# Kernel tuning notes

Measured on AMD Instinct MI355X. Metric: run time of the kernel, lower is better.

The kernel has to match this reference:

```python
import jax, jax.numpy as jnp
import numpy as np

B, N, DIN, D, L, H = 8, 1024, 768, 384, 6, 12
HD = D // H
STD = 0.02
EPS = 1e-5


def setup_inputs() -> dict:
    key = jax.random.key(0)
    ks = jax.random.split(key, 24)
    inp = {}
    inp["x"] = jax.random.normal(ks[0], (B, N, DIN), jnp.float32)
    inp["height_ids"] = jax.random.randint(ks[1], (B, N), 0, 48)
    inp["width_ids"] = jax.random.randint(ks[2], (B, N), 0, 48)
    inp["target_mask"] = jax.random.randint(ks[3], (B, N), 0, 2).astype(bool)
    inp["sequence_ids"] = jnp.sort(jax.random.randint(ks[4], (B, N), 0, 8), axis=-1)
    inp["sequence_mask"] = (jax.random.randint(ks[5], (B, N), 0, 10) > 8)
    inp["r"] = 0
    # parameters (weights stored [in, out]; y = x @ W + b)
    inp["embed_w"] = jax.random.normal(ks[6], (DIN, D), jnp.float32) * STD
    inp["embed_b"] = jnp.zeros((D,), jnp.float32)
    inp["h_embed"] = jax.random.normal(ks[7], (48, D), jnp.float32) * STD
    inp["w_embed"] = jax.random.normal(ks[8], (48, D), jnp.float32) * STD
    inp["mask_token"] = jax.random.normal(ks[9], (D,), jnp.float32) * STD
    rescale = (1.0 / jnp.sqrt(2.0 * (jnp.arange(L) + 1.0))).astype(jnp.float32)
    inp["norm1_w"] = jnp.ones((L, D), jnp.float32)
    inp["norm1_b"] = jnp.zeros((L, D), jnp.float32)
    inp["ls1"] = 1e-5 * jnp.ones((L, D), jnp.float32)
    inp["qkv_w"] = jax.random.normal(ks[10], (L, D, 3 * D), jnp.float32) * STD
    inp["qkv_b"] = jnp.zeros((L, 3 * D), jnp.float32)
    inp["proj_w"] = jax.random.normal(ks[11], (L, D, D), jnp.float32) * STD * rescale[:, None, None]
    inp["proj_b"] = jnp.zeros((L, D), jnp.float32)
    inp["norm2_w"] = jnp.ones((L, D), jnp.float32)
    inp["norm2_b"] = jnp.zeros((L, D), jnp.float32)
    inp["fc1_w"] = jax.random.normal(ks[12], (L, D, 4 * D), jnp.float32) * STD
    inp["fc1_b"] = jnp.zeros((L, 4 * D), jnp.float32)
    inp["fc2_w"] = jax.random.normal(ks[13], (L, 4 * D, D), jnp.float32) * STD * rescale[:, None, None]
    inp["fc2_b"] = jnp.zeros((L, D), jnp.float32)
    inp["ls2"] = 1e-5 * jnp.ones((L, D), jnp.float32)
    inp["pnorm_w"] = jnp.ones((D,), jnp.float32)
    inp["pnorm_b"] = jnp.zeros((D,), jnp.float32)
    inp["pproj_w"] = jax.random.normal(ks[14], (D, DIN), jnp.float32) * STD
    inp["pproj_b"] = jnp.zeros((DIN,), jnp.float32)
    return inp


def _layernorm(x, w, b):
    mu = jnp.mean(x, axis=-1, keepdims=True)
    var = jnp.mean(jnp.square(x - mu), axis=-1, keepdims=True)
    return (x - mu) * jax.lax.rsqrt(var + EPS) * w + b


def _attention(x, attn_mask, qkv_w, qkv_b, proj_w, proj_b):
    # x: [B,N,D]; attn_mask: [B,1,N,N] True where attention is disallowed
    qkv = (x @ qkv_w + qkv_b).reshape(B, N, 3, H, HD).transpose(2, 0, 3, 1, 4)
    q, k, v = qkv[0], qkv[1], qkv[2]  # [B,H,N,HD]
    attn = jnp.einsum("bhnd,bhmd->bhnm", q, k) * (HD ** -0.5)
    neg_inf = jnp.finfo(attn.dtype).min
    attn = jnp.where(attn_mask, neg_inf, attn)
    attn = jax.nn.softmax(attn, axis=-1)
    out = jnp.einsum("bhnm,bhmd->bhnd", attn, v).transpose(0, 2, 1, 3).reshape(B, N, D)
    return out @ proj_w + proj_b


def reference(x, height_ids, width_ids, target_mask, sequence_ids, sequence_mask, r,
              embed_w, embed_b, h_embed, w_embed, mask_token,
              norm1_w, norm1_b, ls1, qkv_w, qkv_b, proj_w, proj_b,
              norm2_w, norm2_b, fc1_w, fc1_b, fc2_w, fc2_b, ls2,
              pnorm_w, pnorm_b, pproj_w, pproj_b):
    h = x @ embed_w + embed_b
    tm = target_mask[..., None]
    h = jnp.where(tm, mask_token, h)
    h = h + h_embed[height_ids] + w_embed[width_ids]
    # packed-sequence block-diagonal mask; True = NOT allowed
    mask = sequence_ids[:, :, None] != sequence_ids[:, None, :]
    mask = mask | sequence_mask[:, :, None] | sequence_mask[:, None, :]
    mask = mask[:, None]  # broadcast over heads: [B,1,N,N]
    for i in range(L):  # r == 0 path: plain blocks, tome is None
        h = h + ls1[i] * _attention(_layernorm(h, norm1_w[i], norm1_b[i]), mask,
                                    qkv_w[i], qkv_b[i], proj_w[i], proj_b[i])
        z = _layernorm(h, norm2_w[i], norm2_b[i])
        z = jax.nn.gelu(z @ fc1_w[i] + fc1_b[i], approximate=False) @ fc2_w[i] + fc2_b[i]
        h = h + ls2[i] * z
    h = _layernorm(h, pnorm_w, pnorm_b)
    return h @ pproj_w + pproj_b
```

## Files before the change

### kernel.cpp

```cpp
#include <hip/hip_runtime.h>
#include <math.h>

#define BB   8
#define NN   1024
#define DIN  768
#define DD   384
#define LL   6
#define HH   12
#define HDD  32
#define MM   (BB*NN)
#define EPSF 1e-5f

typedef __attribute__((ext_vector_type(8))) short short8;
typedef __attribute__((ext_vector_type(4))) float f32x4;

__device__ __forceinline__ unsigned short f2b(float f) {
    unsigned int u = __builtin_bit_cast(unsigned int, f);
    u = (u + 0x7fffu + ((u >> 16) & 1u)) >> 16;
    return (unsigned short)u;
}
__device__ __forceinline__ float b2f(unsigned short h) {
    return __builtin_bit_cast(float, ((unsigned int)h) << 16);
}

__global__ __launch_bounds__(1024) void cvt_mask_k(const void* __restrict__ src,
                                                   int n, int* __restrict__ dst)
{
    __shared__ int flag;
    if (threadIdx.x == 0) flag = 0;
    __syncthreads();
    const int* si = (const int*)src;
    int nq = n >> 2;
    int any = 0;
    for (int i = threadIdx.x; i < nq; i += blockDim.x) any |= si[i] & ~1;
    if (any) atomicOr(&flag, 1);
    __syncthreads();
    if (flag) {
        const unsigned char* sb = (const unsigned char*)src;
        for (int i = threadIdx.x; i < n; i += blockDim.x) dst[i] = sb[i];
    } else {
        for (int i = threadIdx.x; i < n; i += blockDim.x) dst[i] = si[i];
    }
}

__global__ __launch_bounds__(64) void kminmax_k(const int* __restrict__ sids,
                                                const int* __restrict__ smask,
                                                int2* __restrict__ kmm)
{
    int e = blockIdx.x;
    int b = e >> 4, kt = e & 15;
    int lane = threadIdx.x;
    int kk = b * NN + kt * 64 + lane;
    int s = sids[kk];
    int msk = smask[kk];
    int mn = msk ? 0x7fffffff : s;
    int mx = msk ? (int)0x80000000 : s;
    #pragma unroll
    for (int off = 32; off; off >>= 1) {
        mn = min(mn, __shfl_xor(mn, off));
        mx = max(mx, __shfl_xor(mx, off));
    }
    if (lane == 0) kmm[e] = make_int2(mn, mx);
}

__global__ __launch_bounds__(256) void vmean_k(const unsigned short* __restrict__ qkv,
                                               unsigned short* __restrict__ vmean)
{
    __shared__ float part[8][32];
    int bh = blockIdx.x;
    int b = bh / HH, h = bh % HH;
    int d = threadIdx.x & 31, grp = threadIdx.x >> 5;
    const unsigned short* vp = qkv + (size_t)(b * NN + grp * 128) * (3 * DD)
                                   + 2 * DD + h * HDD + d;
    float s = 0.f;
    for (int n = 0; n < 128; ++n)
        s += b2f(vp[(size_t)n * 3 * DD]);
    part[grp][d] = s;
    __syncthreads();
    if (grp == 0) {
        float t = 0.f;
        #pragma unroll
        for (int g2 = 0; g2 < 8; ++g2) t += part[g2][d];
        vmean[bh * HDD + d] = f2b(t * (1.0f / NN));
    }
}

__global__ __launch_bounds__(256) void tcast_k(const float* __restrict__ W,
                                               unsigned short* __restrict__ Wt,
                                               int K, int N)
{
    __shared__ float tile[32][33];
    const size_t lstr = (size_t)K * N;
    const float* Wl = W + blockIdx.z * lstr;
    unsigned short* Wtl = Wt + blockIdx.z * lstr;
    int k0 = blockIdx.x * 32, n0 = blockIdx.y * 32;
    int tx = threadIdx.x & 31, ty = threadIdx.x >> 5;
    #pragma unroll
    for (int r = 0; r < 32; r += 8)
        tile[ty + r][tx] = Wl[(size_t)(k0 + ty + r) * N + n0 + tx];
    __syncthreads();
    #pragma unroll
    for (int r = 0; r < 32; r += 8)
        Wtl[(size_t)(n0 + ty + r) * K + k0 + tx] = f2b(tile[tx][ty + r]);
}

__global__ __launch_bounds__(256) void tcast2_k(const float* __restrict__ W,
                                                unsigned short* __restrict__ WTh,
                                                unsigned short* __restrict__ WTl,
                                                int K, int N)
{
    __shared__ float tile[32][33];
    int k0 = blockIdx.x * 32, n0 = blockIdx.y * 32;
    int tx = threadIdx.x & 31, ty = threadIdx.x >> 5;
    #pragma unroll
    for (int r = 0; r < 32; r += 8)
        tile[ty + r][tx] = W[(size_t)(k0 + ty + r) * N + n0 + tx];
    __syncthreads();
    #pragma unroll
    for (int r = 0; r < 32; r += 8) {
        float v = tile[tx][ty + r];
        unsigned short hi = f2b(v);
        unsigned short lo = f2b(v - b2f(hi));
        size_t idx = (size_t)(n0 + ty + r) * K + k0 + tx;
        WTh[idx] = hi;
        WTl[idx] = lo;
    }
}

template <int EPI>
__global__ __launch_bounds__(256) void sgemm_k(
    const float* __restrict__ A,
    const unsigned short* __restrict__ WTh, const unsigned short* __restrict__ WTl,
    const float* __restrict__ bias, float* __restrict__ out,
    int K, int NO,
    const int* __restrict__ tmask, const int* __restrict__ hids,
    const int* __restrict__ wids, const float* __restrict__ mtok,
    const float* __restrict__ hemb, const float* __restrict__ wemb)
{
    __shared__ unsigned short Ah[128][40];
    __shared__ unsigned short Al[128][40];
    __shared__ unsigned short Bh[64][40];
    __shared__ unsigned short Bl[64][40];

    const int tid  = threadIdx.x;
    const int lane = tid & 63;
    const int wave = tid >> 6;
    const int wr = wave >> 1, wc = wave & 1;
    const int rowBase = blockIdx.x * 128;
    const int colBase = blockIdx.y * 64;
    const int rr = lane & 15;
    const int kr = (lane >> 4) * 8;

    f32x4 acc[4][2] = {};

    for (int k0 = 0; k0 < K; k0 += 32) {
        #pragma unroll
        for (int i = 0; i < 4; ++i) {
            int s   = tid + i * 256;
            int row = s >> 3;
            int q   = (s & 7) * 4;
            float4 av = *(const float4*)&A[(size_t)(rowBase + row) * K + k0 + q];
            ushort4 h4, l4;
            #pragma unroll
            for (int e = 0; e < 4; ++e) {
                float v = ((const float*)&av)[e];
                unsigned short hi = f2b(v);
                ((unsigned short*)&h4)[e] = hi;
                ((unsigned short*)&l4)[e] = f2b(v - b2f(hi));
            }
            *(ushort4*)&Ah[row][q] = h4;
            *(ushort4*)&Al[row][q] = l4;
        }
        {
            int s   = tid;
            int row = s >> 2;
            int seg = (s & 3) * 8;
            size_t gi = (size_t)(colBase + row) * K + k0 + seg;
            *(short8*)&Bh[row][seg] = *(const short8*)&WTh[gi];
            *(short8*)&Bl[row][seg] = *(const short8*)&WTl[gi];
        }
        __syncthreads();

        short8 ah[4], al[4], bh2[2], bl2[2];
        #pragma unroll
        for (int i = 0; i < 4; ++i) {
            ah[i] = *(const short8*)&Ah[wr * 64 + i * 16 + rr][kr];
            al[i] = *(const short8*)&Al[wr * 64 + i * 16 + rr][kr];
        }
        #pragma unroll
        for (int j = 0; j < 2; ++j) {
            bh2[j] = *(const short8*)&Bh[wc * 32 + j * 16 + rr][kr];
            bl2[j] = *(const short8*)&Bl[wc * 32 + j * 16 + rr][kr];
        }
        #pragma unroll
        for (int i = 0; i < 4; ++i)
            #pragma unroll
            for (int j = 0; j < 2; ++j) {
                acc[i][j] = __builtin_amdgcn_mfma_f32_16x16x32_bf16(
                    al[i], bh2[j], acc[i][j], 0, 0, 0);
                acc[i][j] = __builtin_amdgcn_mfma_f32_16x16x32_bf16(
                    ah[i], bl2[j], acc[i][j], 0, 0, 0);
                acc[i][j] = __builtin_amdgcn_mfma_f32_16x16x32_bf16(
                    ah[i], bh2[j], acc[i][j], 0, 0, 0);
            }
        __syncthreads();
    }

    const int colq = colBase + wc * 32 + rr;
    const int rq0  = rowBase + wr * 64 + (lane >> 4) * 4;
    #pragma unroll
    for (int j = 0; j < 2; ++j) {
        const int col = colq + j * 16;
        const float bi = bias[col];
        #pragma unroll
        for (int i = 0; i < 4; ++i) {
            #pragma unroll
            for (int r = 0; r < 4; ++r) {
                const int row = rq0 + i * 16 + r;
                float v = acc[i][j][r] + bi;
                if constexpr (EPI == 1) {
                    float xv = tmask[row] ? mtok[col] : v;
                    out[(size_t)row * NO + col] = xv
                        + hemb[(size_t)hids[row] * DD + col]
                        + wemb[(size_t)wids[row] * DD + col];
                } else {
                    out[(size_t)row * NO + col] = v;
                }
            }
        }
    }
}

template <int EPI>
__global__ __launch_bounds__(256) void bgemm_k(
    const unsigned short* __restrict__ A, const unsigned short* __restrict__ Wt,
    const float* __restrict__ bias, void* __restrict__ out,
    int K, int NO, const float* __restrict__ ls)
{
    __shared__ unsigned short As[128][40];
    __shared__ unsigned short Bs[128][40];

    const int tid  = threadIdx.x;
    const int lane = tid & 63;
    const int wave = tid >> 6;
    const int wr = wave >> 1, wc = wave & 1;
    const int rowBase = blockIdx.x * 128;
    const int colBase = blockIdx.y * 128;
    const int rr = lane & 15;
    const int kr = (lane >> 4) * 8;

    f32x4 acc[4][4] = {};

    for (int k0 = 0; k0 < K; k0 += 32) {
        #pragma unroll
        for (int i = 0; i < 2; ++i) {
            int s   = tid + i * 256;
            int row = s >> 2;
            int seg = (s & 3) * 8;
            *(short8*)&As[row][seg] =
                *(const short8*)&A[(size_t)(rowBase + row) * K + k0 + seg];
            *(short8*)&Bs[row][seg] =
                *(const short8*)&Wt[(size_t)(colBase + row) * K + k0 + seg];
        }
        __syncthreads();

        short8 af[4], bfr[4];
        #pragma unroll
        for (int i = 0; i < 4; ++i)
            af[i] = *(const short8*)&As[wr * 64 + i * 16 + rr][kr];
        #pragma unroll
        for (int j = 0; j < 4; ++j)
            bfr[j] = *(const short8*)&Bs[wc * 64 + j * 16 + rr][kr];
        #pragma unroll
        for (int i = 0; i < 4; ++i)
            #pragma unroll
            for (int j = 0; j < 4; ++j)
                acc[i][j] = __builtin_amdgcn_mfma_f32_16x16x32_bf16(
                    af[i], bfr[j], acc[i][j], 0, 0, 0);
        __syncthreads();
    }

    const int colq = colBase + wc * 64 + rr;
    const int rq0  = rowBase + wr * 64 + (lane >> 4) * 4;
    #pragma unroll
    for (int j = 0; j < 4; ++j) {
        const int col = colq + j * 16;
        const float bi = bias[col];
        float lsv = 0.f;
        if constexpr (EPI == 2) lsv = ls[col];
        #pragma unroll
        for (int i = 0; i < 4; ++i) {
            #pragma unroll
            for (int r = 0; r < 4; ++r) {
                const int row = rq0 + i * 16 + r;
                float v = acc[i][j][r] + bi;
                if constexpr (EPI == 0) {
                    ((unsigned short*)out)[(size_t)row * NO + col] = f2b(v);
                } else if constexpr (EPI == 2) {
                    float* hp = (float*)out + (size_t)row * NO + col;
                    *hp += lsv * v;
                } else {
                    float g = 0.5f * v * (1.0f + erff(v * 0.70710678118654752f));
                    ((unsigned short*)out)[(size_t)row * NO + col] = f2b(g);
                }
            }
        }
    }
}

template <int OUT>
__global__ __launch_bounds__(256) void ln_k(
    const float* __restrict__ X, const float* __restrict__ w,
    const float* __restrict__ b, void* __restrict__ Y)
{
    int row  = blockIdx.x * 4 + (threadIdx.x >> 6);
    int lane = threadIdx.x & 63;
    const float* xr = X + (size_t)row * DD;

    float x[6];
    #pragma unroll
    for (int j = 0; j < 6; ++j) x[j] = xr[lane + 64 * j];

    float s = 0.f;
    #pragma unroll
    for (int j = 0; j < 6; ++j) s += x[j];
    #pragma unroll
    for (int off = 32; off > 0; off >>= 1) s += __shfl_xor(s, off);
    float mu = s * (1.0f / 384.0f);

    float v = 0.f;
    #pragma unroll
    for (int j = 0; j < 6; ++j) { float d = x[j] - mu; v += d * d; }
    #pragma unroll
    for (int off = 32; off > 0; off >>= 1) v += __shfl_xor(v, off);
    float rstd = rsqrtf(v * (1.0f / 384.0f) + EPSF);

    #pragma unroll
    for (int j = 0; j < 6; ++j) {
        int c = lane + 64 * j;
        float y = (x[j] - mu) * rstd * w[c] + b[c];
        if constexpr (OUT == 0) ((float*)Y)[(size_t)row * DD + c] = y;
        else ((unsigned short*)Y)[(size_t)row * DD + c] = f2b(y);
    }
}

__global__ __launch_bounds__(256) void attn_mfma_k(
    const unsigned short* __restrict__ qkv, const int* __restrict__ sids,
    const int* __restrict__ smask, const int2* __restrict__ kmm,
    const unsigned short* __restrict__ vmean, unsigned short* __restrict__ out)
{
    __shared__ unsigned short Vt[32][72];
    __shared__ int ck[64];
    __shared__ unsigned short P[4][16][64];
    __shared__ int qmn[4], qmx[4];

    const int tid  = threadIdx.x;
    const int lane = tid & 63;
    const int wave = tid >> 6;
    const int g = lane >> 4;
    const int c = lane & 15;

    const int bh = blockIdx.x >> 4;
    const int qt = blockIdx.x & 15;
    const int b = bh / HH, h = bh % HH;
    const int q0w = qt * 64 + wave * 16;
    const size_t qrow = 3 * DD;

    const short8 qf = *(const short8*)&qkv[(size_t)(b * NN + q0w + c) * qrow + h * HDD + g * 8];

    int cq[4];
    #pragma unroll
    for (int r = 0; r < 4; ++r) {
        int qq = b * NN + q0w + 4 * g + r;
        cq[r] = smask[qq] ? -2 : sids[qq];
    }

    {
        int lmin = 0x7fffffff, lmax = (int)0x80000000;
        #pragma unroll
        for (int r = 0; r < 4; ++r) {
            if (cq[r] != -2) { lmin = min(lmin, cq[r]); lmax = max(lmax, cq[r]); }
        }
        #pragma unroll
        for (int off = 32; off; off >>= 1) {
            lmin = min(lmin, __shfl_xor(lmin, off));
            lmax = max(lmax, __shfl_xor(lmax, off));
        }
        if (lane == 0) { qmn[wave] = lmin; qmx[wave] = lmax; }
    }
    __syncthreads();
    int qminb = min(min(qmn[0], qmn[1]), min(qmn[2], qmn[3]));
    int qmaxb = max(max(qmx[0], qmx[1]), max(qmx[2], qmx[3]));

    float m[4] = {-INFINITY, -INFINITY, -INFINITY, -INFINITY};
    float l[4] = {};
    f32x4 o[2] = {};
    const f32x4 zero = {};
    const float scale = 0.17677669529663687f;
    const float FMIN = -3.402823466e38f;

    for (int kt = 0; kt < NN / 64; ++kt) {
        const int2 kr = kmm[(b << 4) + kt];
        if (kr.x > qmaxb || kr.y < qminb) continue;

        const int kb = kt * 64;
        {
            int key = tid & 63;
            int d8  = (tid >> 6) * 8;
            short8 v = *(const short8*)&qkv[(size_t)(b * NN + kb + key) * qrow + 2 * DD + h * HDD + d8];
            #pragma unroll
            for (int e = 0; e < 8; ++e)
                Vt[d8 + e][key] = (unsigned short)v[e];
            if (tid < 64) {
                int kk = b * NN + kb + tid;
                ck[tid] = smask[kk] ? -1 : sids[kk];
            }
        }
        __syncthreads();

        f32x4 s4[4];
        #pragma unroll
        for (int j = 0; j < 4; ++j) {
            short8 kf = *(const short8*)&qkv[(size_t)(b * NN + kb + 16 * j + c) * qrow + DD + h * HDD + g * 8];
            s4[j] = __builtin_amdgcn_mfma_f32_16x16x32_bf16(qf, kf, zero, 0, 0, 0);
        }

        float pm[4] = {FMIN, FMIN, FMIN, FMIN};
        #pragma unroll
        for (int j = 0; j < 4; ++j) {
            const int ckj = ck[16 * j + c];
            #pragma unroll
            for (int r = 0; r < 4; ++r) {
                float sv = (cq[r] != ckj) ? FMIN : s4[j][r] * scale;
                s4[j][r] = sv;
                pm[r] = fmaxf(pm[r], sv);
            }
        }
        #pragma unroll
        for (int off = 1; off < 16; off <<= 1)
            #pragma unroll
            for (int r = 0; r < 4; ++r)
                pm[r] = fmaxf(pm[r], __shfl_xor(pm[r], off));

        float fac[4], psum[4];
        #pragma unroll
        for (int r = 0; r < 4; ++r) {
            float mn = fmaxf(m[r], pm[r]);
            fac[r] = __expf(m[r] - mn);
            m[r] = mn;
            psum[r] = 0.f;
        }
        #pragma unroll
        for (int j = 0; j < 4; ++j) {
            #pragma unroll
            for (int r = 0; r < 4; ++r) {
                float p = __expf(s4[j][r] - m[r]);
                psum[r] += p;
                int row  = 4 * g + r;
                int colb = (2 * (16 * j + c)) ^ ((row & 7) << 4);
                *(unsigned short*)((char*)&P[wave][row][0] + colb) = f2b(p);
            }
        }
        #pragma unroll
        for (int off = 1; off < 16; off <<= 1)
            #pragma unroll
            for (int r = 0; r < 4; ++r)
                psum[r] += __shfl_xor(psum[r], off);
        #pragma unroll
        for (int r = 0; r < 4; ++r) l[r] = l[r] * fac[r] + psum[r];

        #pragma unroll
        for (int dc = 0; dc < 2; ++dc)
            #pragma unroll
            for (int r = 0; r < 4; ++r)
                o[dc][r] *= fac[r];

        #pragma unroll
        for (int kc = 0; kc < 2; ++kc) {
            int colb = (2 * (kc * 32 + g * 8)) ^ ((c & 7) << 4);
            short8 pf = *(const short8*)((char*)&P[wave][c][0] + colb);
            #pragma unroll
            for (int dc = 0; dc < 2; ++dc) {
                short8 vf = *(const short8*)&Vt[dc * 16 + c][kc * 32 + g * 8];
                o[dc] = __builtin_amdgcn_mfma_f32_16x16x32_bf16(pf, vf, o[dc], 0, 0, 0);
            }
        }
        __syncthreads();
    }

    #pragma unroll
    for (int r = 0; r < 4; ++r) {
        unsigned short* op = &out[(size_t)(b * NN + q0w + 4 * g + r) * DD + h * HDD];
        if (cq[r] == -2) {
            #pragma unroll
            for (int dc = 0; dc < 2; ++dc)
                op[dc * 16 + c] = vmean[bh * HDD + dc * 16 + c];
        } else {
            const float inv = 1.0f / l[r];
            #pragma unroll
            for (int dc = 0; dc < 2; ++dc)
                op[dc * 16 + c] = f2b(o[dc][r] * inv);
        }
    }
}

extern "C" void kernel_launch(void* const* d_in, const int* in_sizes, int n_in,
                              void* d_out, int out_size, void* d_ws, size_t ws_size,
                              hipStream_t stream)
{
    const float* x        = (const float*)d_in[0];
    const int*   hids     = (const int*)d_in[1];
    const int*   wids     = (const int*)d_in[2];
    const void*  tmask_rw = d_in[3];
    const int*   sids     = (const int*)d_in[4];
    const void*  smask_rw = d_in[5];
    const float* embed_w  = (const float*)d_in[7];
    const float* embed_b  = (const float*)d_in[8];
    const float* h_embed  = (const float*)d_in[9];
    const float* w_embed  = (const float*)d_in[10];
    const float* mtok     = (const float*)d_in[11];
    const float* norm1_w  = (const float*)d_in[12];
    const float* norm1_b  = (const float*)d_in[13];
    const float* ls1      = (const float*)d_in[14];
    const float* qkv_w    = (const float*)d_in[15];
    const float* qkv_b    = (const float*)d_in[16];
    const float* proj_w   = (const float*)d_in[17];
    const float* proj_b   = (const float*)d_in[18];
    const float* norm2_w  = (const float*)d_in[19];
    const float* norm2_b  = (const float*)d_in[20];
    const float* fc1_w    = (const float*)d_in[21];
    const float* fc1_b    = (const float*)d_in[22];
    const float* fc2_w    = (const float*)d_in[23];
    const float* fc2_b    = (const float*)d_in[24];
    const float* ls2      = (const float*)d_in[25];
    const float* pnorm_w  = (const float*)d_in[26];
    const float* pnorm_b  = (const float*)d_in[27];
    const float* pproj_w  = (const float*)d_in[28];
    const float* pproj_b  = (const float*)d_in[29];

    const size_t MD = (size_t)MM * DD;
    float*          h    = (float*)d_ws;
    unsigned short* zb   = (unsigned short*)(h + MD);
    unsigned short* hid  = zb + MD;
    unsigned short* qkvb = hid;
    float*          zf   = (float*)hid;
    unsigned short* wT   = hid + 4 * MD;
    const size_t qkvTsz  = (size_t)LL * 3 * DD * DD;
    const size_t projTsz = (size_t)LL * DD * DD;
    const size_t fc1Tsz  = (size_t)LL * DD * 4 * DD;
    unsigned short* qkvT = wT;
    unsigned short* projT = qkvT + qkvTsz;
    unsigned short* fc1T  = projT + projTsz;
    unsigned short* fc2T  = fc1T + fc1Tsz;
    int* tm32 = (int*)(fc2T + fc1Tsz);
    int* sm32 = tm32 + MM;
    unsigned short* vmean = (unsigned short*)(sm32 + MM);
    int2* kmm = (int2*)(vmean + BB * HH * HDD);
    const size_t ewsz = (size_t)DIN * DD;
    unsigned short* ewT_hi = (unsigned short*)(kmm + BB * 16);
    unsigned short* ewT_lo = ewT_hi + ewsz;
    unsigned short* pwT_hi = ewT_lo + ewsz;
    unsigned short* pwT_lo = pwT_hi + ewsz;

    cvt_mask_k<<<1, 1024, 0, stream>>>(tmask_rw, MM, tm32);
    cvt_mask_k<<<1, 1024, 0, stream>>>(smask_rw, MM, sm32);
    kminmax_k<<<BB * 16, 64, 0, stream>>>(sids, sm32, kmm);

    dim3 t256(256);
    tcast_k<<<dim3(DD/32, 3*DD/32, LL), t256, 0, stream>>>(qkv_w, qkvT, DD, 3*DD);
    tcast_k<<<dim3(DD/32, DD/32,   LL), t256, 0, stream>>>(proj_w, projT, DD, DD);
    tcast_k<<<dim3(DD/32, 4*DD/32, LL), t256, 0, stream>>>(fc1_w, fc1T, DD, 4*DD);
    tcast_k<<<dim3(4*DD/32, DD/32, LL), t256, 0, stream>>>(fc2_w, fc2T, 4*DD, DD);
    tcast2_k<<<dim3(DIN/32, DD/32), t256, 0, stream>>>(embed_w, ewT_hi, ewT_lo, DIN, DD);
    tcast2_k<<<dim3(DD/32, DIN/32), t256, 0, stream>>>(pproj_w, pwT_hi, pwT_lo, DD, DIN);

    sgemm_k<1><<<dim3(MM/128, DD/64), t256, 0, stream>>>(
        x, ewT_hi, ewT_lo, embed_b, h, DIN, DD, tm32, hids, wids, mtok, h_embed, w_embed);

    for (int i = 0; i < LL; ++i) {
        ln_k<1><<<MM/4, t256, 0, stream>>>(h, norm1_w + i*DD, norm1_b + i*DD, zb);
        bgemm_k<0><<<dim3(MM/128, 3*DD/128), t256, 0, stream>>>(
            zb, qkvT + (size_t)i*3*DD*DD, qkv_b + i*3*DD, qkvb, DD, 3*DD, nullptr);
        vmean_k<<<BB * HH, t256, 0, stream>>>(qkvb, vmean);
        attn_mfma_k<<<dim3(BB*HH*(NN/64)), t256, 0, stream>>>(
            qkvb, sids, sm32, kmm, vmean, zb);
        bgemm_k<2><<<dim3(MM/128, DD/128), t256, 0, stream>>>(
            zb, projT + (size_t)i*DD*DD, proj_b + i*DD, h, DD, DD, ls1 + i*DD);
        ln_k<1><<<MM/4, t256, 0, stream>>>(h, norm2_w + i*DD, norm2_b + i*DD, zb);
        bgemm_k<3><<<dim3(MM/128, 4*DD/128), t256, 0, stream>>>(
            zb, fc1T + (size_t)i*DD*4*DD, fc1_b + i*4*DD, hid, DD, 4*DD, nullptr);
        bgemm_k<2><<<dim3(MM/128, DD/128), t256, 0, stream>>>(
            hid, fc2T + (size_t)i*4*DD*DD, fc2_b + i*DD, h, 4*DD, DD, ls2 + i*DD);
    }

    ln_k<0><<<MM/4, t256, 0, stream>>>(h, pnorm_w, pnorm_b, zf);
    sgemm_k<0><<<dim3(MM/128, DIN/64), t256, 0, stream>>>(
        zf, pwT_hi, pwT_lo, pproj_b, (float*)d_out, DD, DIN,
        nullptr, nullptr, nullptr, nullptr, nullptr, nullptr);
}
```

Baseline: 1.289 ms.

## Pre-split fp32 GEMM inputs into bf16 hi/lo planes outside the split GEMM

A new split_k kernel converts the input x into bf16 hi/lo planes once. The final layernorm now writes hi/lo planes directly, so the split-precision sgemm loads pre-split bf16 tiles instead of converting fp32 inside every column block, which repeated the work per column tile. The layernorm is also vectorised to float2 loads and stores. The cost is an extra kernel launch plus an extra pass writing and reading the split x buffers.

```diff
diff --git a/kernel.cpp b/kernel.cpp
--- a/kernel.cpp
+++ b/kernel.cpp
@@ -43,6 +43,28 @@
     }
 }
 
+__global__ __launch_bounds__(256) void split_k(const float* __restrict__ X,
+                                               unsigned short* __restrict__ Xh,
+                                               unsigned short* __restrict__ Xl,
+                                               int n4)
+{
+    int i = blockIdx.x * 256 + threadIdx.x;
+    int stride = gridDim.x * 256;
+    for (; i < n4; i += stride) {
+        float4 v = ((const float4*)X)[i];
+        ushort4 h4, l4;
+        #pragma unroll
+        for (int e = 0; e < 4; ++e) {
+            float f = ((const float*)&v)[e];
+            unsigned short hi = f2b(f);
+            ((unsigned short*)&h4)[e] = hi;
+            ((unsigned short*)&l4)[e] = f2b(f - b2f(hi));
+        }
+        ((ushort4*)Xh)[i] = h4;
+        ((ushort4*)Xl)[i] = l4;
+    }
+}
+
 __global__ __launch_bounds__(64) void kminmax_k(const int* __restrict__ sids,
                                                 const int* __restrict__ smask,
                                                 int2* __restrict__ kmm)
@@ -129,7 +151,7 @@
 
 template <int EPI>
 __global__ __launch_bounds__(256) void sgemm_k(
-    const float* __restrict__ A,
+    const unsigned short* __restrict__ Agh, const unsigned short* __restrict__ Agl,
     const unsigned short* __restrict__ WTh, const unsigned short* __restrict__ WTl,
     const float* __restrict__ bias, float* __restrict__ out,
     int K, int NO,
@@ -155,26 +177,17 @@
 
     for (int k0 = 0; k0 < K; k0 += 32) {
         #pragma unroll
-        for (int i = 0; i < 4; ++i) {
+        for (int i = 0; i < 2; ++i) {
             int s   = tid + i * 256;
-            int row = s >> 3;
-            int q   = (s & 7) * 4;
-            float4 av = *(const float4*)&A[(size_t)(rowBase + row) * K + k0 + q];
-            ushort4 h4, l4;
-            #pragma unroll
-            for (int e = 0; e < 4; ++e) {
-                float v = ((const float*)&av)[e];
-                unsigned short hi = f2b(v);
-                ((unsigned short*)&h4)[e] = hi;
-                ((unsigned short*)&l4)[e] = f2b(v - b2f(hi));
-            }
-            *(ushort4*)&Ah[row][q] = h4;
-            *(ushort4*)&Al[row][q] = l4;
-        }
-        {
-            int s   = tid;
             int row = s >> 2;
             int seg = (s & 3) * 8;
+            size_t gi = (size_t)(rowBase + row) * K + k0 + seg;
+            *(short8*)&Ah[row][seg] = *(const short8*)&Agh[gi];
+            *(short8*)&Al[row][seg] = *(const short8*)&Agl[gi];
+        }
+        {
+            int row = tid >> 2;
+            int seg = (tid & 3) * 8;
             size_t gi = (size_t)(colBase + row) * K + k0 + seg;
             *(short8*)&Bh[row][seg] = *(const short8*)&WTh[gi];
             *(short8*)&Bl[row][seg] = *(const short8*)&WTl[gi];
@@ -311,36 +324,47 @@
 template <int OUT>
 __global__ __launch_bounds__(256) void ln_k(
     const float* __restrict__ X, const float* __restrict__ w,
-    const float* __restrict__ b, void* __restrict__ Y)
+    const float* __restrict__ b, void* __restrict__ Y, void* __restrict__ Yl)
 {
     int row  = blockIdx.x * 4 + (threadIdx.x >> 6);
     int lane = threadIdx.x & 63;
     const float* xr = X + (size_t)row * DD;
 
-    float x[6];
-    #pragma unroll
-    for (int j = 0; j < 6; ++j) x[j] = xr[lane + 64 * j];
+    float2 x2[3];
+    #pragma unroll
+    for (int j = 0; j < 3; ++j)
+        x2[j] = *(const float2*)&xr[2 * (lane + 64 * j)];
 
     float s = 0.f;
     #pragma unroll
-    for (int j = 0; j < 6; ++j) s += x[j];
+    for (int j = 0; j < 3; ++j) s += x2[j].x + x2[j].y;
     #pragma unroll
     for (int off = 32; off > 0; off >>= 1) s += __shfl_xor(s, off);
     float mu = s * (1.0f / 384.0f);
 
     float v = 0.f;
     #pragma unroll
-    for (int j = 0; j < 6; ++j) { float d = x[j] - mu; v += d * d; }
+    for (int j = 0; j < 3; ++j) {
+        float d0 = x2[j].x - mu, d1 = x2[j].y - mu;
+        v += d0 * d0 + d1 * d1;
+    }
     #pragma unroll
     for (int off = 32; off > 0; off >>= 1) v += __shfl_xor(v, off);
     float rstd = rsqrtf(v * (1.0f / 384.0f) + EPSF);
 
     #pragma unroll
-    for (int j = 0; j < 6; ++j) {
-        int c = lane + 64 * j;
-        float y = (x[j] - mu) * rstd * w[c] + b[c];
-        if constexpr (OUT == 0) ((float*)Y)[(size_t)row * DD + c] = y;
-        else ((unsigned short*)Y)[(size_t)row * DD + c] = f2b(y);
+    for (int j = 0; j < 3; ++j) {
+        int c = 2 * (lane + 64 * j);
+        float2 w2 = *(const float2*)&w[c];
+        float2 b2 = *(const float2*)&b[c];
+        float y0 = (x2[j].x - mu) * rstd * w2.x + b2.x;
+        float y1 = (x2[j].y - mu) * rstd * w2.y + b2.y;
+        unsigned short h0 = f2b(y0), h1 = f2b(y1);
+        *(ushort2*)&((unsigned short*)Y)[(size_t)row * DD + c] = make_ushort2(h0, h1);
+        if constexpr (OUT == 2) {
+            unsigned short l0 = f2b(y0 - b2f(h0)), l1 = f2b(y1 - b2f(h1));
+            *(ushort2*)&((unsigned short*)Yl)[(size_t)row * DD + c] = make_ushort2(l0, l1);
+        }
     }
 }
 
@@ -400,8 +424,8 @@
     const float FMIN = -3.402823466e38f;
 
     for (int kt = 0; kt < NN / 64; ++kt) {
-        const int2 kr = kmm[(b << 4) + kt];
-        if (kr.x > qmaxb || kr.y < qminb) continue;
+        const int2 kr2 = kmm[(b << 4) + kt];
+        if (kr2.x > qmaxb || kr2.y < qminb) continue;
 
         const int kb = kt * 64;
         {
@@ -543,7 +567,11 @@
     unsigned short* zb   = (unsigned short*)(h + MD);
     unsigned short* hid  = zb + MD;
     unsigned short* qkvb = hid;
-    float*          zf   = (float*)hid;
+    unsigned short* zfh  = hid;
+    unsigned short* zfl  = hid + MD;
+    const size_t xsz = (size_t)MM * DIN;
+    unsigned short* xh = hid;
+    unsigned short* xl = hid + xsz;
     unsigned short* wT   = hid + 4 * MD;
     const size_t qkvTsz  = (size_t)LL * 3 * DD * DD;
     const size_t projTsz = (size_t)LL * DD * DD;
@@ -573,12 +601,13 @@
     tcast_k<<<dim3(4*DD/32, DD/32, LL), t256, 0, stream>>>(fc2_w, fc2T, 4*DD, DD);
     tcast2_k<<<dim3(DIN/32, DD/32), t256, 0, stream>>>(embed_w, ewT_hi, ewT_lo, DIN, DD);
     tcast2_k<<<dim3(DD/32, DIN/32), t256, 0, stream>>>(pproj_w, pwT_hi, pwT_lo, DD, DIN);
+    split_k<<<2048, t256, 0, stream>>>(x, xh, xl, (int)(xsz / 4));
 
     sgemm_k<1><<<dim3(MM/128, DD/64), t256, 0, stream>>>(
-        x, ewT_hi, ewT_lo, embed_b, h, DIN, DD, tm32, hids, wids, mtok, h_embed, w_embed);
+        xh, xl, ewT_hi, ewT_lo, embed_b, h, DIN, DD, tm32, hids, wids, mtok, h_embed, w_embed);
 
     for (int i = 0; i < LL; ++i) {
-        ln_k<1><<<MM/4, t256, 0, stream>>>(h, norm1_w + i*DD, norm1_b + i*DD, zb);
+        ln_k<1><<<MM/4, t256, 0, stream>>>(h, norm1_w + i*DD, norm1_b + i*DD, zb, nullptr);
         bgemm_k<0><<<dim3(MM/128, 3*DD/128), t256, 0, stream>>>(
             zb, qkvT + (size_t)i*3*DD*DD, qkv_b + i*3*DD, qkvb, DD, 3*DD, nullptr);
         vmean_k<<<BB * HH, t256, 0, stream>>>(qkvb, vmean);
@@ -586,15 +615,15 @@
             qkvb, sids, sm32, kmm, vmean, zb);
         bgemm_k<2><<<dim3(MM/128, DD/128), t256, 0, stream>>>(
             zb, projT + (size_t)i*DD*DD, proj_b + i*DD, h, DD, DD, ls1 + i*DD);
-        ln_k<1><<<MM/4, t256, 0, stream>>>(h, norm2_w + i*DD, norm2_b + i*DD, zb);
+        ln_k<1><<<MM/4, t256, 0, stream>>>(h, norm2_w + i*DD, norm2_b + i*DD, zb, nullptr);
         bgemm_k<3><<<dim3(MM/128, 4*DD/128), t256, 0, stream>>>(
             zb, fc1T + (size_t)i*DD*4*DD, fc1_b + i*4*DD, hid, DD, 4*DD, nullptr);
         bgemm_k<2><<<dim3(MM/128, DD/128), t256, 0, stream>>>(
             hid, fc2T + (size_t)i*4*DD*DD, fc2_b + i*DD, h, 4*DD, DD, ls2 + i*DD);
     }
 
-    ln_k<0><<<MM/4, t256, 0, stream>>>(h, pnorm_w, pnorm_b, zf);
+    ln_k<2><<<MM/4, t256, 0, stream>>>(h, pnorm_w, pnorm_b, zfh, zfl);
     sgemm_k<0><<<dim3(MM/128, DIN/64), t256, 0, stream>>>(
-        zf, pwT_hi, pwT_lo, pproj_b, (float*)d_out, DD, DIN,
+        zfh, zfl, pwT_hi, pwT_lo, pproj_b, (float*)d_out, DD, DIN,
         nullptr, nullptr, nullptr, nullptr, nullptr, nullptr);
 }
```

New measurement: 1.292 ms. About the same (+0.2%).
